# Optimization experiments

Hardware: AMD Instinct MI355X
Metric: run time of the kernel (lower is better)

The kernel has to match this reference:

```python
import jax, jax.numpy as jnp
import numpy as np
import math

EMBED_DIM = 1024
MEMORY_DIM = 1024
MEMORY_SIZE = 2048
B, S = 8, 4096


def bitnet_linear(x, W, b):
    """Eval-mode BitNetLinear: 1.58-bit weight quant + 8-bit activation quant."""
    w_scale = jnp.mean(jnp.abs(W))
    qW = jnp.sign(W) * (jnp.abs(W) > 0.5 * w_scale).astype(W.dtype)
    i_scale = jnp.max(jnp.abs(x)) / 127.0
    qx = jnp.clip(jnp.round(x / i_scale), -128.0, 127.0)
    out = jnp.einsum('bsi,oi->bso', qx, qW) * (w_scale * i_scale)
    return out + b


def setup_inputs() -> dict:
    key = jax.random.key(0)
    ks = jax.random.split(key, 9)
    return {
        'x': jax.random.normal(ks[0], (B, S, EMBED_DIM), jnp.float32),
        'memory_keys': jax.random.normal(ks[1], (MEMORY_SIZE, MEMORY_DIM), jnp.float32),
        'memory_values': jax.random.normal(ks[2], (MEMORY_SIZE, EMBED_DIM), jnp.float32),
        'Wk': jax.random.normal(ks[3], (MEMORY_DIM, EMBED_DIM), jnp.float32) * 0.1,
        'bk': jnp.zeros((MEMORY_DIM,), jnp.float32),
        'Wv': jax.random.normal(ks[4], (EMBED_DIM, EMBED_DIM), jnp.float32) * 0.1,
        'bv': jnp.zeros((EMBED_DIM,), jnp.float32),
        'Wo': jax.random.normal(ks[5], (EMBED_DIM, EMBED_DIM), jnp.float32) * 0.1,
        'bo': jnp.zeros((EMBED_DIM,), jnp.float32),
    }


def reference(x, memory_keys, memory_values, Wk, bk, Wv, bv, Wo, bo):
    # quantized key/value projections
    query_keys = bitnet_linear(x, Wk, bk)          # [B, S, Dm]
    _query_values = bitnet_linear(x, Wv, bv)       # computed in original (used only by update path)
    # memory cross-attention over fixed bank
    similarities = jnp.einsum('bsd,md->bsm', query_keys, memory_keys)  # [B, S, M]
    attention_weights = jax.nn.softmax(similarities / math.sqrt(MEMORY_DIM), axis=-1)
    retrieved = jnp.einsum('bsm,me->bse', attention_weights, memory_values)  # [B, S, E]
    output = bitnet_linear(x + retrieved, Wo, bo)
    return output
```

## Files before the change

kernel.cpp:

```cpp
#include <hip/hip_runtime.h>
#include <hip/hip_bf16.h>
#include <stdint.h>

typedef __attribute__((ext_vector_type(8))) short bf16x8;
typedef __attribute__((ext_vector_type(4))) float f32x4;
typedef __attribute__((ext_vector_type(4))) int i32x4;

#define BM 128
#define BN 128
#define BK 64

struct Scalars {
  double sum_wk;
  double sum_wo;
  unsigned int max_x_bits;
  unsigned int max_y_bits;
};

__device__ __forceinline__ unsigned short f2bf(float f) {
  __hip_bfloat16 h = __float2bfloat16(f);
  return *reinterpret_cast<unsigned short*>(&h);
}

__device__ __forceinline__ void async16(void* lds, const void* g) {
  __builtin_amdgcn_global_load_lds((__attribute__((address_space(1))) void*)g,
                                   (__attribute__((address_space(3))) void*)lds, 16, 0, 0);
}

__device__ __forceinline__ void tile_swizzle(int nxShift, int& bx, int& by) {
  const int per = gridDim.x >> 3;
  const int tile = (blockIdx.x & 7) * per + (blockIdx.x >> 3);
  bx = tile & ((1 << nxShift) - 1);
  by = tile >> nxShift;
}

__global__ __launch_bounds__(256) void abssum_kernel(const float* __restrict__ w, size_t n,
                                                     double* __restrict__ out) {
  size_t tid = (size_t)blockIdx.x * blockDim.x + threadIdx.x;
  size_t stride = (size_t)gridDim.x * blockDim.x;
  double s = 0.0;
  for (size_t i = tid * 4; i < n; i += stride * 4) {
    float4 v = *(const float4*)(w + i);
    s += (double)fabsf(v.x) + (double)fabsf(v.y) + (double)fabsf(v.z) + (double)fabsf(v.w);
  }
#pragma unroll
  for (int o = 32; o > 0; o >>= 1) s += __shfl_xor(s, o);
  __shared__ double sm[4];
  if ((threadIdx.x & 63) == 0) sm[threadIdx.x >> 6] = s;
  __syncthreads();
  if (threadIdx.x == 0) atomicAdd(out, sm[0] + sm[1] + sm[2] + sm[3]);
}

__global__ __launch_bounds__(256) void absmax_kernel(const float* __restrict__ x, size_t n,
                                                     unsigned int* __restrict__ out) {
  size_t tid = (size_t)blockIdx.x * blockDim.x + threadIdx.x;
  size_t stride = (size_t)gridDim.x * blockDim.x;
  float m = 0.0f;
  for (size_t i = tid * 4; i < n; i += stride * 4) {
    float4 v = *(const float4*)(x + i);
    m = fmaxf(m, fmaxf(fmaxf(fabsf(v.x), fabsf(v.y)), fmaxf(fabsf(v.z), fabsf(v.w))));
  }
#pragma unroll
  for (int o = 32; o > 0; o >>= 1) m = fmaxf(m, __shfl_xor(m, o));
  __shared__ float sm[4];
  if ((threadIdx.x & 63) == 0) sm[threadIdx.x >> 6] = m;
  __syncthreads();
  if (threadIdx.x == 0)
    atomicMax(out, __float_as_uint(fmaxf(fmaxf(sm[0], sm[1]), fmaxf(sm[2], sm[3]))));
}

__global__ __launch_bounds__(256) void quant_act_i8_kernel(const float* __restrict__ x,
                                                           char* __restrict__ q,
                                                           const unsigned int* __restrict__ maxbits,
                                                           size_t n) {
  const float isc = __uint_as_float(*maxbits) / 127.0f;
  size_t tid = (size_t)blockIdx.x * blockDim.x + threadIdx.x;
  size_t stride = (size_t)gridDim.x * blockDim.x;
  for (size_t i = tid * 4; i < n; i += stride * 4) {
    float4 v = *(const float4*)(x + i);
    char4 o;
    o.x = (char)(int)fminf(fmaxf(rintf(v.x / isc), -128.f), 127.f);
    o.y = (char)(int)fminf(fmaxf(rintf(v.y / isc), -128.f), 127.f);
    o.z = (char)(int)fminf(fmaxf(rintf(v.z / isc), -128.f), 127.f);
    o.w = (char)(int)fminf(fmaxf(rintf(v.w / isc), -128.f), 127.f);
    *(char4*)(q + i) = o;
  }
}

__global__ __launch_bounds__(256) void quant_w_i8_kernel(const float* __restrict__ W,
                                                         char* __restrict__ qW,
                                                         const double* __restrict__ sum, size_t n) {
  const float wsc = (float)(*sum / (double)n);
  const float thr = 0.5f * wsc;
  size_t tid = (size_t)blockIdx.x * blockDim.x + threadIdx.x;
  size_t stride = (size_t)gridDim.x * blockDim.x;
  for (size_t i = tid * 4; i < n; i += stride * 4) {
    float4 v = *(const float4*)(W + i);
    char4 o;
    o.x = (char)(fabsf(v.x) > thr ? (v.x > 0.f ? 1 : -1) : 0);
    o.y = (char)(fabsf(v.y) > thr ? (v.y > 0.f ? 1 : -1) : 0);
    o.z = (char)(fabsf(v.z) > thr ? (v.z > 0.f ? 1 : -1) : 0);
    o.w = (char)(fabsf(v.w) > thr ? (v.w > 0.f ? 1 : -1) : 0);
    *(char4*)(qW + i) = o;
  }
}

__global__ __launch_bounds__(256) void cast_bf16_kernel(const float* __restrict__ src,
                                                        __hip_bfloat16* __restrict__ dst,
                                                        size_t n) {
  size_t tid = (size_t)blockIdx.x * blockDim.x + threadIdx.x;
  size_t stride = (size_t)gridDim.x * blockDim.x;
  for (size_t i = tid * 4; i < n; i += stride * 4) {
    float4 v = *(const float4*)(src + i);
    ushort4 o;
    o.x = f2bf(v.x); o.y = f2bf(v.y); o.z = f2bf(v.z); o.w = f2bf(v.w);
    *(ushort4*)((unsigned short*)dst + i) = o;
  }
}

__global__ void transpose_mv_kernel(const float* __restrict__ mv,
                                    __hip_bfloat16* __restrict__ mvT) {
  __shared__ float tile[32][33];
  int tx = threadIdx.x, ty = threadIdx.y;
  int e = blockIdx.x * 32 + tx;
  int m = blockIdx.y * 32 + ty;
  tile[ty][tx] = mv[(size_t)m * 1024 + e];
  __syncthreads();
  int om = blockIdx.y * 32 + tx;
  mvT[(size_t)(blockIdx.x * 32 + ty) * 2048 + om] = __float2bfloat16(tile[tx][ty]);
}

__global__ __launch_bounds__(256) void softmax_kernel(__hip_bfloat16* __restrict__ sims) {
  unsigned short* row = (unsigned short*)(sims + (size_t)blockIdx.x * 2048);
  const int t = threadIdx.x;
  const int l = t & 63, wv = t >> 6;
  uint4 r4 = *(const uint4*)(row + t * 8);
  float v[8];
  v[0] = __uint_as_float(r4.x << 16); v[1] = __uint_as_float(r4.x & 0xffff0000u);
  v[2] = __uint_as_float(r4.y << 16); v[3] = __uint_as_float(r4.y & 0xffff0000u);
  v[4] = __uint_as_float(r4.z << 16); v[5] = __uint_as_float(r4.z & 0xffff0000u);
  v[6] = __uint_as_float(r4.w << 16); v[7] = __uint_as_float(r4.w & 0xffff0000u);
  float m = v[0];
#pragma unroll
  for (int i = 1; i < 8; ++i) m = fmaxf(m, v[i]);
#pragma unroll
  for (int o = 32; o > 0; o >>= 1) m = fmaxf(m, __shfl_xor(m, o));
  __shared__ float red[4], red2[4];
  if (l == 0) red[wv] = m;
  __syncthreads();
  m = fmaxf(fmaxf(red[0], red[1]), fmaxf(red[2], red[3]));
  float s = 0.f;
#pragma unroll
  for (int i = 0; i < 8; ++i) { v[i] = expf(v[i] - m); s += v[i]; }
#pragma unroll
  for (int o = 32; o > 0; o >>= 1) s += __shfl_xor(s, o);
  if (l == 0) red2[wv] = s;
  __syncthreads();
  s = red2[0] + red2[1] + red2[2] + red2[3];
  unsigned short b[8];
#pragma unroll
  for (int i = 0; i < 8; ++i) b[i] = f2bf(v[i] / s);
  uint4 o4;
  o4.x = (unsigned)b[0] | ((unsigned)b[1] << 16);
  o4.y = (unsigned)b[2] | ((unsigned)b[3] << 16);
  o4.z = (unsigned)b[4] | ((unsigned)b[5] << 16);
  o4.w = (unsigned)b[6] | ((unsigned)b[7] << 16);
  *(uint4*)(row + t * 8) = o4;
}

template <int EPI>
__global__ __launch_bounds__(256) void gemm_bt(
    const __hip_bfloat16* __restrict__ A, const __hip_bfloat16* __restrict__ B,
    void* __restrict__ C, const float* __restrict__ Xadd,
    Scalars* __restrict__ sc, int Ndim, int Kdim, int nxShift) {
  __shared__ __hip_bfloat16 sA[BM * BK];
  __shared__ __hip_bfloat16 sB[BN * BK];
  __shared__ float wred[4];

  int bx, by;
  tile_swizzle(nxShift, bx, by);
  const int rowBlk = by * BM;
  const int colBlk = bx * BN;

  const int t = threadIdx.x;
  const int w = t >> 6;
  const int l = t & 63;
  const int wm = w >> 1, wn = w & 1;
  const int quad = l >> 4;
  const int m16 = l & 15;
  const int rIn = l >> 3;
  const int dIn = (l & 7) ^ rIn;

  f32x4 acc[4][4] = {};

  for (int kb = 0; kb < Kdim; kb += BK) {
#pragma unroll
    for (int i = 0; i < 4; ++i) {
      const int c = w + 4 * i;
      const int r = 8 * c + rIn;
      async16(&sA[c * 512], A + (size_t)(rowBlk + r) * Kdim + kb + dIn * 8);
      async16(&sB[c * 512], B + (size_t)(colBlk + r) * Kdim + kb + dIn * 8);
    }
    __syncthreads();

#pragma unroll
    for (int ks = 0; ks < 2; ++ks) {
      bf16x8 af[4], bfr[4];
#pragma unroll
      for (int i = 0; i < 4; ++i) {
        const int r = wm * 64 + i * 16 + m16;
        const int p = (ks * 4 + quad) ^ (r & 7);
        af[i] = *(const bf16x8*)(&sA[r * 64 + p * 8]);
      }
#pragma unroll
      for (int j = 0; j < 4; ++j) {
        const int r = wn * 64 + j * 16 + m16;
        const int p = (ks * 4 + quad) ^ (r & 7);
        bfr[j] = *(const bf16x8*)(&sB[r * 64 + p * 8]);
      }
#pragma unroll
      for (int i = 0; i < 4; ++i)
#pragma unroll
        for (int j = 0; j < 4; ++j)
          acc[i][j] = __builtin_amdgcn_mfma_f32_16x16x32_bf16(af[i], bfr[j], acc[i][j], 0, 0, 0);
    }
    __syncthreads();
  }

  float amax = 0.0f;
#pragma unroll
  for (int i = 0; i < 4; ++i) {
#pragma unroll
    for (int j = 0; j < 4; ++j) {
      const int col = colBlk + wn * 64 + j * 16 + m16;
#pragma unroll
      for (int rg = 0; rg < 4; ++rg) {
        const int row = rowBlk + wm * 64 + i * 16 + quad * 4 + rg;
        float v = acc[i][j][rg];
        if (EPI == 1) {
          ((__hip_bfloat16*)C)[(size_t)row * Ndim + col] = __float2bfloat16(v * 0.03125f);
        } else {
          v += Xadd[(size_t)row * Ndim + col];
          ((float*)C)[(size_t)row * Ndim + col] = v;
          amax = fmaxf(amax, fabsf(v));
        }
      }
    }
  }

  if (EPI == 2) {
#pragma unroll
    for (int o = 32; o > 0; o >>= 1) amax = fmaxf(amax, __shfl_xor(amax, o));
    if (l == 0) wred[w] = amax;
    __syncthreads();
    if (t == 0)
      atomicMax(&sc->max_y_bits,
                __float_as_uint(fmaxf(fmaxf(wred[0], wred[1]), fmaxf(wred[2], wred[3]))));
  }
}

template <int EPI>
__global__ __launch_bounds__(256) void gemm_i8(
    const char* __restrict__ A, const char* __restrict__ B, void* __restrict__ C,
    const float* __restrict__ bias, Scalars* __restrict__ sc,
    int Ndim, int Kdim, int nxShift) {
  __shared__ char sA[BM * 128];
  __shared__ char sB[BN * 128];

  int bx, by;
  tile_swizzle(nxShift, bx, by);
  const int rowBlk = by * BM;
  const int colBlk = bx * BN;

  const int t = threadIdx.x;
  const int w = t >> 6;
  const int l = t & 63;
  const int wm = w >> 1, wn = w & 1;
  const int quad = l >> 4;
  const int m16 = l & 15;
  const int rIn = l >> 3;
  const int dIn = (l & 7) ^ rIn;

  i32x4 acc[4][4] = {};

  for (int kb = 0; kb < Kdim; kb += 128) {
#pragma unroll
    for (int i = 0; i < 4; ++i) {
      const int c = w + 4 * i;
      const int r = 8 * c + rIn;
      async16(&sA[c * 1024], A + (size_t)(rowBlk + r) * Kdim + kb + dIn * 16);
      async16(&sB[c * 1024], B + (size_t)(colBlk + r) * Kdim + kb + dIn * 16);
    }
    __syncthreads();

#pragma unroll
    for (int ks = 0; ks < 2; ++ks) {
      i32x4 af[4], bfr[4];
#pragma unroll
      for (int i = 0; i < 4; ++i) {
        const int r = wm * 64 + i * 16 + m16;
        const int p = (ks * 4 + quad) ^ (r & 7);
        af[i] = *(const i32x4*)(&sA[r * 128 + p * 16]);
      }
#pragma unroll
      for (int j = 0; j < 4; ++j) {
        const int r = wn * 64 + j * 16 + m16;
        const int p = (ks * 4 + quad) ^ (r & 7);
        bfr[j] = *(const i32x4*)(&sB[r * 128 + p * 16]);
      }
#pragma unroll
      for (int i = 0; i < 4; ++i)
#pragma unroll
        for (int j = 0; j < 4; ++j)
          acc[i][j] = __builtin_amdgcn_mfma_i32_16x16x64_i8(af[i], bfr[j], acc[i][j], 0, 0, 0);
    }
    __syncthreads();
  }

  float s;
  if (EPI == 0) {
    s = (float)(sc->sum_wk * (1.0 / 1048576.0)) * (__uint_as_float(sc->max_x_bits) / 127.0f);
  } else {
    s = (float)(sc->sum_wo * (1.0 / 1048576.0)) * (__uint_as_float(sc->max_y_bits) / 127.0f);
  }

#pragma unroll
  for (int i = 0; i < 4; ++i) {
#pragma unroll
    for (int j = 0; j < 4; ++j) {
      const int col = colBlk + wn * 64 + j * 16 + m16;
#pragma unroll
      for (int rg = 0; rg < 4; ++rg) {
        const int row = rowBlk + wm * 64 + i * 16 + quad * 4 + rg;
        const float v = (float)acc[i][j][rg] * s + bias[col];
        if (EPI == 0)
          ((__hip_bfloat16*)C)[(size_t)row * Ndim + col] = __float2bfloat16(v);
        else
          ((float*)C)[(size_t)row * Ndim + col] = v;
      }
    }
  }
}

extern "C" void kernel_launch(void* const* d_in, const int* in_sizes, int n_in,
                              void* d_out, int out_size, void* d_ws, size_t ws_size,
                              hipStream_t stream) {
  (void)in_sizes; (void)n_in; (void)out_size; (void)ws_size;
  const float* x  = (const float*)d_in[0];
  const float* mk = (const float*)d_in[1];
  const float* mv = (const float*)d_in[2];
  const float* Wk = (const float*)d_in[3];
  const float* bk = (const float*)d_in[4];
  const float* Wo = (const float*)d_in[7];
  const float* bo = (const float*)d_in[8];
  float* out = (float*)d_out;

  const int M = 32768, E = 1024, MEM = 2048;

  char* ws = (char*)d_ws;
  Scalars* sc = (Scalars*)ws;
  const size_t off0 = 256;
  char* qx8 = ws + off0;
  __hip_bfloat16* qk = (__hip_bfloat16*)(ws + off0 + (size_t)M * E);
  float* y = (float*)(ws + off0);
  const size_t off1 = off0 + (size_t)M * E * 4;
  __hip_bfloat16* sims = (__hip_bfloat16*)(ws + off1);
  char* qy8 = (char*)sims;
  const size_t off2 = off1 + (size_t)M * MEM * 2;
  char* qWk8 = ws + off2;
  char* qWo8 = qWk8 + (size_t)E * E;
  __hip_bfloat16* mkb = (__hip_bfloat16*)(qWo8 + (size_t)E * E);
  __hip_bfloat16* mvT = mkb + (size_t)MEM * E;

  hipMemsetAsync(ws, 0, 256, stream);

  abssum_kernel<<<dim3(256), dim3(256), 0, stream>>>(Wk, (size_t)E * E, &sc->sum_wk);
  abssum_kernel<<<dim3(256), dim3(256), 0, stream>>>(Wo, (size_t)E * E, &sc->sum_wo);
  absmax_kernel<<<dim3(2048), dim3(256), 0, stream>>>(x, (size_t)M * E, &sc->max_x_bits);

  quant_act_i8_kernel<<<dim3(2048), dim3(256), 0, stream>>>(x, qx8, &sc->max_x_bits, (size_t)M * E);
  quant_w_i8_kernel<<<dim3(256), dim3(256), 0, stream>>>(Wk, qWk8, &sc->sum_wk, (size_t)E * E);
  quant_w_i8_kernel<<<dim3(256), dim3(256), 0, stream>>>(Wo, qWo8, &sc->sum_wo, (size_t)E * E);
  cast_bf16_kernel<<<dim3(256), dim3(256), 0, stream>>>(mk, mkb, (size_t)MEM * E);
  transpose_mv_kernel<<<dim3(E / 32, MEM / 32), dim3(32, 32), 0, stream>>>(mv, mvT);

  gemm_i8<0><<<dim3((E / BN) * (M / BM)), dim3(256), 0, stream>>>(qx8, qWk8, qk, bk, sc, E, E, 3);
  gemm_bt<1><<<dim3((MEM / BN) * (M / BM)), dim3(256), 0, stream>>>(qk, mkb, sims, nullptr, sc, MEM, E, 4);
  softmax_kernel<<<dim3(M), dim3(256), 0, stream>>>(sims);
  gemm_bt<2><<<dim3((E / BN) * (M / BM)), dim3(256), 0, stream>>>(sims, mvT, y, x, sc, E, MEM, 3);
  quant_act_i8_kernel<<<dim3(2048), dim3(256), 0, stream>>>(y, qy8, &sc->max_y_bits, (size_t)M * E);
  gemm_i8<1><<<dim3((E / BN) * (M / BM)), dim3(256), 0, stream>>>(qy8, qWo8, out, bo, sc, E, E, 3);
}
```

Before: 864.4 us.

## Replace bf16 GEMMs with 256x256 double-buffered 8-wave pipelined kernel

The two bf16 GEMMs (query-keys times memory keys, and attention weights times memory values) move from a 128x128 tile, 4-wave, single-buffered loop to a 256x256 tile with 8 waves. The new loop double-buffers LDS and splits each K-step into four phases that interleave async global-to-LDS staging with MFMA bursts. It uses explicit vmcnt/lgkmcnt waits, raw barriers and s_setprio to overlap memory with compute. This aims to hide load latency and raise data reuse per tile, at the cost of much higher register and LDS pressure (128KB LDS per block) and fragile hand-written synchronisation.

Result: faster. 769.7 us (-11.0%).

```diff
diff --git a/kernel.cpp b/kernel.cpp
--- a/kernel.cpp
+++ b/kernel.cpp
@@ -168,75 +168,127 @@
   *(uint4*)(row + t * 8) = o4;
 }
 
+#define CFENCE() asm volatile("" ::: "memory")
+#define BAR8() { CFENCE(); __builtin_amdgcn_s_barrier(); CFENCE(); }
+#define WLGKM0() { asm volatile("s_waitcnt lgkmcnt(0)" ::: "memory"); __builtin_amdgcn_sched_barrier(0); }
+#define WVM(N) asm volatile("s_waitcnt vmcnt(" #N ")" ::: "memory")
+
 template <int EPI>
-__global__ __launch_bounds__(256) void gemm_bt(
+__global__ __launch_bounds__(512, 2) void gemm_bt8(
     const __hip_bfloat16* __restrict__ A, const __hip_bfloat16* __restrict__ B,
     void* __restrict__ C, const float* __restrict__ Xadd,
     Scalars* __restrict__ sc, int Ndim, int Kdim, int nxShift) {
-  __shared__ __hip_bfloat16 sA[BM * BK];
-  __shared__ __hip_bfloat16 sB[BN * BK];
-  __shared__ float wred[4];
+  __shared__ __align__(16) char sm[2][4][16384];
 
   int bx, by;
   tile_swizzle(nxShift, bx, by);
-  const int rowBlk = by * BM;
-  const int colBlk = bx * BN;
+  const int rowBlk = by * 256;
+  const int colBlk = bx * 256;
 
   const int t = threadIdx.x;
-  const int w = t >> 6;
-  const int l = t & 63;
-  const int wm = w >> 1, wn = w & 1;
-  const int quad = l >> 4;
-  const int m16 = l & 15;
-  const int rIn = l >> 3;
-  const int dIn = (l & 7) ^ rIn;
-
-  f32x4 acc[4][4] = {};
-
-  for (int kb = 0; kb < Kdim; kb += BK) {
-#pragma unroll
-    for (int i = 0; i < 4; ++i) {
-      const int c = w + 4 * i;
-      const int r = 8 * c + rIn;
-      async16(&sA[c * 512], A + (size_t)(rowBlk + r) * Kdim + kb + dIn * 8);
-      async16(&sB[c * 512], B + (size_t)(colBlk + r) * Kdim + kb + dIn * 8);
-    }
-    __syncthreads();
-
-#pragma unroll
-    for (int ks = 0; ks < 2; ++ks) {
-      bf16x8 af[4], bfr[4];
-#pragma unroll
-      for (int i = 0; i < 4; ++i) {
-        const int r = wm * 64 + i * 16 + m16;
-        const int p = (ks * 4 + quad) ^ (r & 7);
-        af[i] = *(const bf16x8*)(&sA[r * 64 + p * 8]);
-      }
-#pragma unroll
-      for (int j = 0; j < 4; ++j) {
-        const int r = wn * 64 + j * 16 + m16;
-        const int p = (ks * 4 + quad) ^ (r & 7);
-        bfr[j] = *(const bf16x8*)(&sB[r * 64 + p * 8]);
-      }
-#pragma unroll
-      for (int i = 0; i < 4; ++i)
-#pragma unroll
-        for (int j = 0; j < 4; ++j)
-          acc[i][j] = __builtin_amdgcn_mfma_f32_16x16x32_bf16(af[i], bfr[j], acc[i][j], 0, 0, 0);
-    }
-    __syncthreads();
+  const int w = t >> 6, l = t & 63;
+  const int wm = w >> 2, wn = w & 3;
+  const int quad = l >> 4, m16 = l & 15;
+
+  const int NT = Kdim >> 6;
+  const int NIT = NT >> 1;
+
+#define STAGE_A8(slot, half, tk)                                                          \
+  if ((tk) < NT) {                                                                        \
+    _Pragma("unroll") for (int j = 0; j < 2; ++j) {                                       \
+      const int idx = j * 64 + (t >> 3);                                                  \
+      const int kby = (((t & 7) ^ (idx & 7)) << 4);                                       \
+      const size_t gr = (size_t)(rowBlk + ((idx >> 6) << 7) + ((half) << 6) + (idx & 63));\
+      async16(&sm[slot][half][j * 8192 + (w << 10)],                                      \
+              (const char*)A + (gr * (size_t)Kdim + ((size_t)(tk) << 6)) * 2 + kby);      \
+    }                                                                                     \
+  }
+
+#define STAGE_B8(slot, half, tk)                                                          \
+  if ((tk) < NT) {                                                                        \
+    _Pragma("unroll") for (int j = 0; j < 2; ++j) {                                       \
+      const int idx = j * 64 + (t >> 3);                                                  \
+      const int kby = (((t & 7) ^ (idx & 7)) << 4);                                       \
+      const size_t gr = (size_t)(colBlk + ((idx >> 5) << 6) + ((half) << 5) + (idx & 31));\
+      async16(&sm[slot][2 + (half)][j * 8192 + (w << 10)],                                \
+              (const char*)B + (gr * (size_t)Kdim + ((size_t)(tk) << 6)) * 2 + kby);      \
+    }                                                                                     \
+  }
+
+#define LDA8(dst, slot, f, ks)                                                            \
+  dst = *(const bf16x8*)&sm[slot][(f) >> 2][(wm * 64 + ((f)&3) * 16 + m16) * 128 +        \
+        ((((ks) << 6) + (quad << 4)) ^ ((m16 & 7) << 4))];
+
+#define LDB8(dst, slot, g, ks)                                                            \
+  dst = *(const bf16x8*)&sm[slot][2 + ((g) >> 1)][(wn * 32 + ((g)&1) * 16 + m16) * 128 +  \
+        ((((ks) << 6) + (quad << 4)) ^ ((m16 & 7) << 4))];
+
+#define PHASE_MFMA(FO, GO, BREG)                                                          \
+  __builtin_amdgcn_s_setprio(1);                                                          \
+  _Pragma("unroll") for (int f = 0; f < 4; ++f)                                           \
+    _Pragma("unroll") for (int g = 0; g < 2; ++g) {                                       \
+      acc[(FO) + f][(GO) + g] = __builtin_amdgcn_mfma_f32_16x16x32_bf16(                  \
+          af[f][0], BREG[g][0], acc[(FO) + f][(GO) + g], 0, 0, 0);                        \
+      acc[(FO) + f][(GO) + g] = __builtin_amdgcn_mfma_f32_16x16x32_bf16(                  \
+          af[f][1], BREG[g][1], acc[(FO) + f][(GO) + g], 0, 0, 0);                        \
+    }                                                                                     \
+  __builtin_amdgcn_s_setprio(0);
+
+#define TILE_STEP8(s, tk, last)                                                           \
+  {                                                                                       \
+                            \
+    _Pragma("unroll") for (int f = 0; f < 4; ++f) { LDA8(af[f][0], s, f, 0); LDA8(af[f][1], s, f, 1); } \
+    _Pragma("unroll") for (int g = 0; g < 2; ++g) { LDB8(b0[g][0], s, g, 0); LDB8(b0[g][1], s, g, 1); } \
+    STAGE_A8((s) ^ 1, 1, (tk) + 1);                                                       \
+    BAR8(); WLGKM0();                                                                     \
+    PHASE_MFMA(0, 0, b0);                                                                 \
+    BAR8();                                                                               \
+           \
+    _Pragma("unroll") for (int g = 0; g < 2; ++g) { LDB8(b1[g][0], s, 2 + g, 0); LDB8(b1[g][1], s, 2 + g, 1); } \
+    STAGE_A8(s, 0, (tk) + 2);                                                             \
+    BAR8(); WLGKM0();                                                                     \
+    PHASE_MFMA(0, 2, b1);                                                                 \
+    BAR8();                                                                               \
+                       \
+    _Pragma("unroll") for (int f = 0; f < 4; ++f) { LDA8(af[f][0], s, 4 + f, 0); LDA8(af[f][1], s, 4 + f, 1); } \
+    STAGE_B8(s, 0, (tk) + 2);                                                             \
+    BAR8(); WLGKM0();                                                                     \
+    PHASE_MFMA(4, 2, b1);                                                                 \
+    BAR8();                                                                               \
+        \
+    STAGE_B8(s, 1, (tk) + 2);                                                             \
+    if (last) { WVM(0); } else { WVM(6); }                                                \
+    BAR8();                                                                               \
+    PHASE_MFMA(4, 0, b0);                                                                 \
+    BAR8();                                                                               \
+  }
+
+  bf16x8 af[4][2], b0[2][2], b1[2][2];
+  f32x4 acc[8][4] = {};
+
+  STAGE_A8(0, 0, 0); STAGE_B8(0, 0, 0); STAGE_B8(0, 1, 0); STAGE_A8(0, 1, 0);
+  CFENCE();
+  STAGE_A8(1, 0, 1); STAGE_B8(1, 0, 1); STAGE_B8(1, 1, 1);
+  WVM(6);
+  BAR8();
+
+  for (int it = 0; it < NIT; ++it) {
+    const int tk = it * 2;
+    const bool last = (it == NIT - 1);
+    TILE_STEP8(0, tk, last);
+    TILE_STEP8(1, tk + 1, last);
   }
 
   float amax = 0.0f;
 #pragma unroll
-  for (int i = 0; i < 4; ++i) {
-#pragma unroll
-    for (int j = 0; j < 4; ++j) {
-      const int col = colBlk + wn * 64 + j * 16 + m16;
+  for (int f = 0; f < 8; ++f) {
+#pragma unroll
+    for (int g = 0; g < 4; ++g) {
+      const int col = colBlk + wn * 64 + g * 16 + m16;
 #pragma unroll
       for (int rg = 0; rg < 4; ++rg) {
-        const int row = rowBlk + wm * 64 + i * 16 + quad * 4 + rg;
-        float v = acc[i][j][rg];
+        const int row = rowBlk + wm * 128 + f * 16 + quad * 4 + rg;
+        float v = acc[f][g][rg];
         if (EPI == 1) {
           ((__hip_bfloat16*)C)[(size_t)row * Ndim + col] = __float2bfloat16(v * 0.03125f);
         } else {
@@ -249,14 +301,24 @@
   }
 
   if (EPI == 2) {
+    __shared__ float wred[8];
 #pragma unroll
     for (int o = 32; o > 0; o >>= 1) amax = fmaxf(amax, __shfl_xor(amax, o));
     if (l == 0) wred[w] = amax;
     __syncthreads();
-    if (t == 0)
-      atomicMax(&sc->max_y_bits,
-                __float_as_uint(fmaxf(fmaxf(wred[0], wred[1]), fmaxf(wred[2], wred[3]))));
-  }
+    if (t == 0) {
+      float m = wred[0];
+#pragma unroll
+      for (int i = 1; i < 8; ++i) m = fmaxf(m, wred[i]);
+      atomicMax(&sc->max_y_bits, __float_as_uint(m));
+    }
+  }
+#undef STAGE_A8
+#undef STAGE_B8
+#undef LDA8
+#undef LDB8
+#undef PHASE_MFMA
+#undef TILE_STEP8
 }
 
 template <int EPI>
@@ -385,9 +447,9 @@
   transpose_mv_kernel<<<dim3(E / 32, MEM / 32), dim3(32, 32), 0, stream>>>(mv, mvT);
 
   gemm_i8<0><<<dim3((E / BN) * (M / BM)), dim3(256), 0, stream>>>(qx8, qWk8, qk, bk, sc, E, E, 3);
-  gemm_bt<1><<<dim3((MEM / BN) * (M / BM)), dim3(256), 0, stream>>>(qk, mkb, sims, nullptr, sc, MEM, E, 4);
+  gemm_bt8<1><<<dim3((MEM / 256) * (M / 256)), dim3(512), 0, stream>>>(qk, mkb, sims, nullptr, sc, MEM, E, 3);
   softmax_kernel<<<dim3(M), dim3(256), 0, stream>>>(sims);
-  gemm_bt<2><<<dim3((E / BN) * (M / BM)), dim3(256), 0, stream>>>(sims, mvT, y, x, sc, E, MEM, 3);
+  gemm_bt8<2><<<dim3((E / 256) * (M / 256)), dim3(512), 0, stream>>>(sims, mvT, y, x, sc, E, MEM, 2);
   quant_act_i8_kernel<<<dim3(2048), dim3(256), 0, stream>>>(y, qy8, &sc->max_y_bits, (size_t)M * E);
   gemm_i8<1><<<dim3((E / BN) * (M / BM)), dim3(256), 0, stream>>>(qy8, qWo8, out, bo, sc, E, E, 3);
 }
```

## Replace GEMMs with unified 256x256 8-wave double-buffered pipelined kernel

Applied to the files above, without the earlier changes.

Replaces both the bf16 and the int8 GEMM kernels with a single templated 256x256-tile kernel using 512 threads. It double-buffers LDS in halves, interleaves async global-to-LDS loads with MFMA groups under manual barriers and waitcnts, and raises wave priority around the MFMAs. The aim is to hide memory latency and raise per-block data reuse for the four large GEMMs. In exchange it needs much more LDS and registers per block, which lowers occupancy, and the hand-written waitcnt schedule is fragile.

Measured after the change: 774.4 us. 1.12x faster.

```diff
diff --git a/kernel.cpp b/kernel.cpp
--- a/kernel.cpp
+++ b/kernel.cpp
@@ -1,14 +1,11 @@
 #include <hip/hip_runtime.h>
 #include <hip/hip_bf16.h>
 #include <stdint.h>
+#include <type_traits>
 
 typedef __attribute__((ext_vector_type(8))) short bf16x8;
 typedef __attribute__((ext_vector_type(4))) float f32x4;
 typedef __attribute__((ext_vector_type(4))) int i32x4;
-
-#define BM 128
-#define BN 128
-#define BK 64
 
 struct Scalars {
   double sum_wk;
@@ -32,6 +29,13 @@
   const int tile = (blockIdx.x & 7) * per + (blockIdx.x >> 3);
   bx = tile & ((1 << nxShift) - 1);
   by = tile >> nxShift;
+}
+
+__device__ __forceinline__ f32x4 mm(bf16x8 a, bf16x8 b, f32x4 c) {
+  return __builtin_amdgcn_mfma_f32_16x16x32_bf16(a, b, c, 0, 0, 0);
+}
+__device__ __forceinline__ i32x4 mm(i32x4 a, i32x4 b, i32x4 c) {
+  return __builtin_amdgcn_mfma_i32_16x16x64_i8(a, b, c, 0, 0, 0);
 }
 
 __global__ __launch_bounds__(256) void abssum_kernel(const float* __restrict__ w, size_t n,
@@ -168,178 +172,182 @@
   *(uint4*)(row + t * 8) = o4;
 }
 
+#define CFENCE() asm volatile("" ::: "memory")
+#define BAR8() { CFENCE(); __builtin_amdgcn_s_barrier(); CFENCE(); }
+#define WLGKM(N) { asm volatile("s_waitcnt lgkmcnt(" #N ")" ::: "memory"); __builtin_amdgcn_sched_barrier(0); }
+#define WVM(N) asm volatile("s_waitcnt vmcnt(" #N ")" ::: "memory")
+
 template <int EPI>
-__global__ __launch_bounds__(256) void gemm_bt(
-    const __hip_bfloat16* __restrict__ A, const __hip_bfloat16* __restrict__ B,
-    void* __restrict__ C, const float* __restrict__ Xadd,
-    Scalars* __restrict__ sc, int Ndim, int Kdim, int nxShift) {
-  __shared__ __hip_bfloat16 sA[BM * BK];
-  __shared__ __hip_bfloat16 sB[BN * BK];
-  __shared__ float wred[4];
+__global__ __launch_bounds__(512, 2) void gemm8(
+    const char* __restrict__ A, const char* __restrict__ B, void* __restrict__ C,
+    const float* __restrict__ aux, Scalars* __restrict__ sc,
+    int Ndim, int KB, int nxShift) {
+  constexpr bool I8 = (EPI >= 3);
+  using FR  = typename std::conditional<I8, i32x4, bf16x8>::type;
+  using ACC = typename std::conditional<I8, i32x4, f32x4>::type;
+  __shared__ __align__(16) char lds[4][2][16384];
 
   int bx, by;
   tile_swizzle(nxShift, bx, by);
-  const int rowBlk = by * BM;
-  const int colBlk = bx * BN;
-
-  const int t = threadIdx.x;
-  const int w = t >> 6;
-  const int l = t & 63;
-  const int wm = w >> 1, wn = w & 1;
-  const int quad = l >> 4;
-  const int m16 = l & 15;
-  const int rIn = l >> 3;
-  const int dIn = (l & 7) ^ rIn;
-
-  f32x4 acc[4][4] = {};
-
-  for (int kb = 0; kb < Kdim; kb += BK) {
-#pragma unroll
-    for (int i = 0; i < 4; ++i) {
-      const int c = w + 4 * i;
-      const int r = 8 * c + rIn;
-      async16(&sA[c * 512], A + (size_t)(rowBlk + r) * Kdim + kb + dIn * 8);
-      async16(&sB[c * 512], B + (size_t)(colBlk + r) * Kdim + kb + dIn * 8);
+  const int rowBlk = by * 256, colBlk = bx * 256;
+
+  const int t = threadIdx.x, w = t >> 6, l = t & 63;
+  const int wm = w >> 2, wn = w & 3;
+  const int quad = l >> 4, m16 = l & 15;
+  const int NT = KB >> 7, NIT = NT >> 1;
+
+  int voA[2][2], voB[2][2];
+#pragma unroll
+  for (int hf = 0; hf < 2; ++hf)
+#pragma unroll
+    for (int j = 0; j < 2; ++j) {
+      const int idx = j * 64 + (t >> 3);
+      const int kby = ((t & 7) ^ (idx & 7)) << 4;
+      voA[hf][j] = (rowBlk + ((idx >> 6) << 7) + (hf << 6) + (idx & 63)) * KB + kby;
+      voB[hf][j] = (colBlk + ((idx >> 5) << 6) + (hf << 5) + (idx & 31)) * KB + kby;
     }
-    __syncthreads();
-
-#pragma unroll
-    for (int ks = 0; ks < 2; ++ks) {
-      bf16x8 af[4], bfr[4];
-#pragma unroll
-      for (int i = 0; i < 4; ++i) {
-        const int r = wm * 64 + i * 16 + m16;
-        const int p = (ks * 4 + quad) ^ (r & 7);
-        af[i] = *(const bf16x8*)(&sA[r * 64 + p * 8]);
-      }
-#pragma unroll
-      for (int j = 0; j < 4; ++j) {
-        const int r = wn * 64 + j * 16 + m16;
-        const int p = (ks * 4 + quad) ^ (r & 7);
-        bfr[j] = *(const bf16x8*)(&sB[r * 64 + p * 8]);
-      }
-#pragma unroll
-      for (int i = 0; i < 4; ++i)
-#pragma unroll
-        for (int j = 0; j < 4; ++j)
-          acc[i][j] = __builtin_amdgcn_mfma_f32_16x16x32_bf16(af[i], bfr[j], acc[i][j], 0, 0, 0);
-    }
-    __syncthreads();
-  }
+
+  const char* baA[2];
+  const char* baB[2];
+#pragma unroll
+  for (int ks = 0; ks < 2; ++ks) {
+    const int x16 = ((ks << 6) + (quad << 4)) ^ ((m16 & 7) << 4);
+    baA[ks] = &lds[0][0][(wm * 64 + m16) * 128 + x16];
+    baB[ks] = &lds[2][0][(wn * 32 + m16) * 128 + x16];
+  }
+
+#define STG_A(slot, hf, tk)                                                         \
+  if ((tk) < NT) {                                                                  \
+    _Pragma("unroll") for (int j = 0; j < 2; ++j)                                   \
+      async16(&lds[hf][slot][j * 8192 + (w << 10)],                                 \
+              A + (((size_t)(tk)) << 7) + voA[hf][j]);                              \
+  }
+#define STG_B(slot, hf, tk)                                                         \
+  if ((tk) < NT) {                                                                  \
+    _Pragma("unroll") for (int j = 0; j < 2; ++j)                                   \
+      async16(&lds[2 + (hf)][slot][j * 8192 + (w << 10)],                           \
+              B + (((size_t)(tk)) << 7) + voB[hf][j]);                              \
+  }
+
+#define LD_A(dst, slot, hf, f, ks) \
+  dst = *(const FR*)(baA[ks] + ((hf)*32768 + (slot)*16384 + (f)*2048));
+#define LD_B(dst, slot, hf, gg, ks) \
+  dst = *(const FR*)(baB[ks] + ((hf)*32768 + (slot)*16384 + (gg)*2048));
+
+#define R_A0(s) { _Pragma("unroll") for (int f_ = 0; f_ < 4; ++f_) { LD_A(af[f_][0], s, 0, f_, 0); LD_A(af[f_][1], s, 0, f_, 1); } }
+#define R_A1(s) { _Pragma("unroll") for (int f_ = 0; f_ < 4; ++f_) { LD_A(af[f_][0], s, 1, f_, 0); LD_A(af[f_][1], s, 1, f_, 1); } }
+#define R_B0(s) { _Pragma("unroll") for (int g_ = 0; g_ < 2; ++g_) { LD_B(b0[g_][0], s, 0, g_, 0); LD_B(b0[g_][1], s, 0, g_, 1); } }
+#define R_B1(s) { _Pragma("unroll") for (int g_ = 0; g_ < 2; ++g_) { LD_B(b1[g_][0], s, 1, g_, 0); LD_B(b1[g_][1], s, 1, g_, 1); } }
+
+#define MM8(FO, GO, BR)                                                             \
+  __builtin_amdgcn_s_setprio(1);                                                    \
+  _Pragma("unroll") for (int f_ = 0; f_ < 4; ++f_)                                  \
+    _Pragma("unroll") for (int g_ = 0; g_ < 2; ++g_) {                              \
+      acc[(FO) + f_][(GO) + g_] = mm(af[f_][0], BR[g_][0], acc[(FO) + f_][(GO) + g_]); \
+      acc[(FO) + f_][(GO) + g_] = mm(af[f_][1], BR[g_][1], acc[(FO) + f_][(GO) + g_]); \
+    }                                                                               \
+  __builtin_amdgcn_s_setprio(0);
+
+#define TSTEP(s, tk, last)                                                          \
+  {                                                                                 \
+                     \
+    R_B1(s);                                                                        \
+    STG_A((s) ^ 1, 1, (tk) + 1);                                                    \
+    BAR8(); WLGKM(4);                                                               \
+    MM8(0, 0, b0);                                                                  \
+    BAR8();                                                                         \
+        \
+    STG_A(s, 0, (tk) + 2);                                                          \
+    BAR8(); WLGKM(0);                                                               \
+    MM8(0, 2, b1);                                                                  \
+    R_A1(s);                                                                        \
+    BAR8();                                                                         \
+                                                                \
+    STG_B(s, 0, (tk) + 2);                                                          \
+    BAR8(); WLGKM(0);                                                               \
+    MM8(4, 0, b0);                                                                  \
+    BAR8();                                                                         \
+           \
+    STG_B(s, 1, (tk) + 2);                                                          \
+    if (last) { WVM(0); } else { WVM(6); }                                          \
+    BAR8();                                                                         \
+    MM8(4, 2, b1);                                                                  \
+    R_A0((s) ^ 1);                                                                  \
+    R_B0((s) ^ 1);                                                                  \
+    BAR8();                                                                         \
+  }
+
+  FR af[4][2], b0[2][2], b1[2][2];
+  ACC acc[8][4] = {};
+
+  STG_A(0, 0, 0); STG_B(0, 0, 0); STG_B(0, 1, 0); STG_A(0, 1, 0);
+  CFENCE();
+  STG_A(1, 0, 1); STG_B(1, 0, 1); STG_B(1, 1, 1);
+  WVM(6);
+  BAR8();
+  R_A0(0); R_B0(0);
+
+  for (int it = 0; it < NIT; ++it) {
+    const bool last = (it == NIT - 1);
+    TSTEP(0, it * 2, last);
+    TSTEP(1, it * 2 + 1, last);
+  }
+
+  float sK = 0.0f;
+  if constexpr (EPI == 3)
+    sK = (float)(sc->sum_wk * (1.0 / 1048576.0)) * (__uint_as_float(sc->max_x_bits) / 127.0f);
+  if constexpr (EPI == 4)
+    sK = (float)(sc->sum_wo * (1.0 / 1048576.0)) * (__uint_as_float(sc->max_y_bits) / 127.0f);
 
   float amax = 0.0f;
 #pragma unroll
-  for (int i = 0; i < 4; ++i) {
-#pragma unroll
-    for (int j = 0; j < 4; ++j) {
-      const int col = colBlk + wn * 64 + j * 16 + m16;
+  for (int f = 0; f < 8; ++f) {
+#pragma unroll
+    for (int g = 0; g < 4; ++g) {
+      const int col = colBlk + wn * 64 + g * 16 + m16;
 #pragma unroll
       for (int rg = 0; rg < 4; ++rg) {
-        const int row = rowBlk + wm * 64 + i * 16 + quad * 4 + rg;
-        float v = acc[i][j][rg];
-        if (EPI == 1) {
-          ((__hip_bfloat16*)C)[(size_t)row * Ndim + col] = __float2bfloat16(v * 0.03125f);
-        } else {
-          v += Xadd[(size_t)row * Ndim + col];
+        const int row = rowBlk + wm * 128 + f * 16 + quad * 4 + rg;
+        if constexpr (EPI == 1) {
+          ((__hip_bfloat16*)C)[(size_t)row * Ndim + col] =
+              __float2bfloat16(acc[f][g][rg] * 0.03125f);
+        } else if constexpr (EPI == 2) {
+          float v = acc[f][g][rg] + aux[(size_t)row * Ndim + col];
           ((float*)C)[(size_t)row * Ndim + col] = v;
           amax = fmaxf(amax, fabsf(v));
+        } else if constexpr (EPI == 3) {
+          ((__hip_bfloat16*)C)[(size_t)row * Ndim + col] =
+              __float2bfloat16((float)acc[f][g][rg] * sK + aux[col]);
+        } else {
+          ((float*)C)[(size_t)row * Ndim + col] = (float)acc[f][g][rg] * sK + aux[col];
         }
       }
     }
   }
 
-  if (EPI == 2) {
+  if constexpr (EPI == 2) {
+    __shared__ float wred[8];
 #pragma unroll
     for (int o = 32; o > 0; o >>= 1) amax = fmaxf(amax, __shfl_xor(amax, o));
     if (l == 0) wred[w] = amax;
     __syncthreads();
-    if (t == 0)
-      atomicMax(&sc->max_y_bits,
-                __float_as_uint(fmaxf(fmaxf(wred[0], wred[1]), fmaxf(wred[2], wred[3]))));
-  }
-}
-
-template <int EPI>
-__global__ __launch_bounds__(256) void gemm_i8(
-    const char* __restrict__ A, const char* __restrict__ B, void* __restrict__ C,
-    const float* __restrict__ bias, Scalars* __restrict__ sc,
-    int Ndim, int Kdim, int nxShift) {
-  __shared__ char sA[BM * 128];
-  __shared__ char sB[BN * 128];
-
-  int bx, by;
-  tile_swizzle(nxShift, bx, by);
-  const int rowBlk = by * BM;
-  const int colBlk = bx * BN;
-
-  const int t = threadIdx.x;
-  const int w = t >> 6;
-  const int l = t & 63;
-  const int wm = w >> 1, wn = w & 1;
-  const int quad = l >> 4;
-  const int m16 = l & 15;
-  const int rIn = l >> 3;
-  const int dIn = (l & 7) ^ rIn;
-
-  i32x4 acc[4][4] = {};
-
-  for (int kb = 0; kb < Kdim; kb += 128) {
-#pragma unroll
-    for (int i = 0; i < 4; ++i) {
-      const int c = w + 4 * i;
-      const int r = 8 * c + rIn;
-      async16(&sA[c * 1024], A + (size_t)(rowBlk + r) * Kdim + kb + dIn * 16);
-      async16(&sB[c * 1024], B + (size_t)(colBlk + r) * Kdim + kb + dIn * 16);
+    if (t == 0) {
+      float m = wred[0];
+#pragma unroll
+      for (int i = 1; i < 8; ++i) m = fmaxf(m, wred[i]);
+      atomicMax(&sc->max_y_bits, __float_as_uint(m));
     }
-    __syncthreads();
-
-#pragma unroll
-    for (int ks = 0; ks < 2; ++ks) {
-      i32x4 af[4], bfr[4];
-#pragma unroll
-      for (int i = 0; i < 4; ++i) {
-        const int r = wm * 64 + i * 16 + m16;
-        const int p = (ks * 4 + quad) ^ (r & 7);
-        af[i] = *(const i32x4*)(&sA[r * 128 + p * 16]);
-      }
-#pragma unroll
-      for (int j = 0; j < 4; ++j) {
-        const int r = wn * 64 + j * 16 + m16;
-        const int p = (ks * 4 + quad) ^ (r & 7);
-        bfr[j] = *(const i32x4*)(&sB[r * 128 + p * 16]);
-      }
-#pragma unroll
-      for (int i = 0; i < 4; ++i)
-#pragma unroll
-        for (int j = 0; j < 4; ++j)
-          acc[i][j] = __builtin_amdgcn_mfma_i32_16x16x64_i8(af[i], bfr[j], acc[i][j], 0, 0, 0);
-    }
-    __syncthreads();
-  }
-
-  float s;
-  if (EPI == 0) {
-    s = (float)(sc->sum_wk * (1.0 / 1048576.0)) * (__uint_as_float(sc->max_x_bits) / 127.0f);
-  } else {
-    s = (float)(sc->sum_wo * (1.0 / 1048576.0)) * (__uint_as_float(sc->max_y_bits) / 127.0f);
-  }
-
-#pragma unroll
-  for (int i = 0; i < 4; ++i) {
-#pragma unroll
-    for (int j = 0; j < 4; ++j) {
-      const int col = colBlk + wn * 64 + j * 16 + m16;
-#pragma unroll
-      for (int rg = 0; rg < 4; ++rg) {
-        const int row = rowBlk + wm * 64 + i * 16 + quad * 4 + rg;
-        const float v = (float)acc[i][j][rg] * s + bias[col];
-        if (EPI == 0)
-          ((__hip_bfloat16*)C)[(size_t)row * Ndim + col] = __float2bfloat16(v);
-        else
-          ((float*)C)[(size_t)row * Ndim + col] = v;
-      }
-    }
-  }
+  }
+#undef STG_A
+#undef STG_B
+#undef LD_A
+#undef LD_B
+#undef R_A0
+#undef R_A1
+#undef R_B0
+#undef R_B1
+#undef MM8
+#undef TSTEP
 }
 
 extern "C" void kernel_launch(void* const* d_in, const int* in_sizes, int n_in,
@@ -384,10 +392,14 @@
   cast_bf16_kernel<<<dim3(256), dim3(256), 0, stream>>>(mk, mkb, (size_t)MEM * E);
   transpose_mv_kernel<<<dim3(E / 32, MEM / 32), dim3(32, 32), 0, stream>>>(mv, mvT);
 
-  gemm_i8<0><<<dim3((E / BN) * (M / BM)), dim3(256), 0, stream>>>(qx8, qWk8, qk, bk, sc, E, E, 3);
-  gemm_bt<1><<<dim3((MEM / BN) * (M / BM)), dim3(256), 0, stream>>>(qk, mkb, sims, nullptr, sc, MEM, E, 4);
+  gemm8<3><<<dim3((E / 256) * (M / 256)), dim3(512), 0, stream>>>(
+      qx8, qWk8, qk, bk, sc, E, E, 2);
+  gemm8<1><<<dim3((MEM / 256) * (M / 256)), dim3(512), 0, stream>>>(
+      (const char*)qk, (const char*)mkb, sims, nullptr, sc, MEM, 2 * E, 3);
   softmax_kernel<<<dim3(M), dim3(256), 0, stream>>>(sims);
-  gemm_bt<2><<<dim3((E / BN) * (M / BM)), dim3(256), 0, stream>>>(sims, mvT, y, x, sc, E, MEM, 3);
+  gemm8<2><<<dim3((E / 256) * (M / 256)), dim3(512), 0, stream>>>(
+      (const char*)sims, (const char*)mvT, y, x, sc, E, 2 * MEM, 2);
   quant_act_i8_kernel<<<dim3(2048), dim3(256), 0, stream>>>(y, qy8, &sc->max_y_bits, (size_t)M * E);
-  gemm_i8<1><<<dim3((E / BN) * (M / BM)), dim3(256), 0, stream>>>(qy8, qWo8, out, bo, sc, E, E, 3);
-}
+  gemm8<4><<<dim3((E / 256) * (M / 256)), dim3(512), 0, stream>>>(
+      qy8, qWo8, out, bo, sc, E, E, 2);
+}
```
